# Kernel tuning notes

Hardware: AMD Instinct MI355X
Metric: run time of the kernel (lower is better)

The kernel has to match this reference:

```python
import jax, jax.numpy as jnp
import numpy as np

D_MODEL = 1024
NUM_HEADS = 16
HEAD_DIM = D_MODEL // NUM_HEADS  # 64
ROPE_BASE = 10000.0


def setup_inputs() -> dict:
    key = jax.random.key(0)
    ks = jax.random.split(key, 12)
    B, S, D = 4, 2048, D_MODEL
    scale = 1.0 / np.sqrt(D)
    inp = {
        'query': jax.random.normal(ks[0], (B, S, D), jnp.float32),
        'key': jax.random.normal(ks[1], (B, S, D), jnp.float32),
        'value': jax.random.normal(ks[2], (B, S, D), jnp.float32),
        'Wq': jax.random.normal(ks[3], (D, D), jnp.float32) * scale,
        'bq': jnp.zeros((D,), jnp.float32),
        'Wk': jax.random.normal(ks[4], (D, D), jnp.float32) * scale,
        'bk': jnp.zeros((D,), jnp.float32),
        'Wv': jax.random.normal(ks[5], (D, D), jnp.float32) * scale,
        'bv': jnp.zeros((D,), jnp.float32),
        'Wo': jax.random.normal(ks[6], (D, D), jnp.float32) * scale,
        'bo': jnp.zeros((D,), jnp.float32),
    }
    return inp


def _rope_cos_sin(seq_len, head_dim, dtype):
    inv_freq = 1.0 / (ROPE_BASE ** (jnp.arange(0, head_dim, 2, dtype=jnp.float32) / head_dim))
    t = jnp.arange(seq_len, dtype=jnp.float32)
    freqs = jnp.einsum('i,j->ij', t, inv_freq)          # [S, hd/2]
    emb = jnp.concatenate([freqs, freqs], axis=-1)      # [S, hd]
    return jnp.cos(emb).astype(dtype), jnp.sin(emb).astype(dtype)


def _rotate_half(x):
    x1, x2 = jnp.split(x, 2, axis=-1)
    return jnp.concatenate([-x2, x1], axis=-1)


def reference(query, key, value, Wq, bq, Wk, bk, Wv, bv, Wo, bo):
    B, T, D = query.shape
    H, hd = NUM_HEADS, HEAD_DIM
    # projections -> [B, H, S, hd]
    Q = (query @ Wq + bq).reshape(B, T, H, hd).transpose(0, 2, 1, 3)
    K = (key @ Wk + bk).reshape(B, -1, H, hd).transpose(0, 2, 1, 3)
    V = (value @ Wv + bv).reshape(B, -1, H, hd).transpose(0, 2, 1, 3)
    # RoPE
    cos, sin = _rope_cos_sin(T, hd, Q.dtype)            # [S, hd]
    Q = Q * cos + _rotate_half(Q) * sin
    K = K * cos + _rotate_half(K) * sin
    # attention
    scores = jnp.einsum('bhtd,bhsd->bhts', Q, K) / jnp.sqrt(jnp.asarray(hd, Q.dtype))
    attn = jax.nn.softmax(scores, axis=-1)
    context = jnp.einsum('bhts,bhsd->bhtd', attn, V)
    context = context.transpose(0, 2, 1, 3).reshape(B, T, D)
    return context @ Wo + bo
```

## Files before the change

### kernel.cpp

```cpp
#include <hip/hip_runtime.h>
#include <hip/hip_bf16.h>
#include <cstdint>
#include <cstddef>

typedef __bf16 bf16_t;
typedef __bf16 bf16x8 __attribute__((ext_vector_type(8)));
typedef __bf16 bf16x4v __attribute__((ext_vector_type(4)));
typedef __bf16 bf16x2v __attribute__((ext_vector_type(2)));
typedef float f32x4 __attribute__((ext_vector_type(4)));
typedef float f32x16 __attribute__((ext_vector_type(16)));
typedef uint32_t u32x4 __attribute__((ext_vector_type(4)));
typedef uint32_t u32x2 __attribute__((ext_vector_type(2)));

#define DEVI static __device__ __forceinline__

DEVI void gl_lds16(const void* g, void* l) {
    __builtin_amdgcn_global_load_lds((const __attribute__((address_space(1))) void*)g,
                                     (__attribute__((address_space(3))) void*)l, 16, 0, 0);
}

DEVI float fexp2(float x) {
#if __has_builtin(__builtin_amdgcn_exp2f)
    return __builtin_amdgcn_exp2f(x);
#else
    return __expf(x * 0.6931471805599453f);
#endif
}

DEVI uint32_t pkbf16(float a, float b) {
    bf16x2v t;
    t[0] = (bf16_t)a;
    t[1] = (bf16_t)b;
    return __builtin_bit_cast(uint32_t, t);
}

__global__ __launch_bounds__(256) void castk(const float* __restrict__ i0, const float* __restrict__ i1,
                                             const float* __restrict__ i2, bf16_t* __restrict__ o0,
                                             bf16_t* __restrict__ o1, bf16_t* __restrict__ o2) {
    const float* in = blockIdx.y == 0 ? i0 : blockIdx.y == 1 ? i1 : i2;
    bf16_t* out = blockIdx.y == 0 ? o0 : blockIdx.y == 1 ? o1 : o2;
    size_t i = ((size_t)blockIdx.x * 256 + threadIdx.x) * 4;
    float4 v = *(const float4*)(in + i);
    bf16x4v o;
    o[0] = (bf16_t)v.x; o[1] = (bf16_t)v.y; o[2] = (bf16_t)v.z; o[3] = (bf16_t)v.w;
    *(bf16x4v*)(out + i) = o;
}

__global__ __launch_bounds__(256) void wtrans(const float* __restrict__ W0, const float* __restrict__ W1,
                                              const float* __restrict__ W2, const float* __restrict__ W3,
                                              bf16_t* __restrict__ O0, bf16_t* __restrict__ O1,
                                              bf16_t* __restrict__ O2, bf16_t* __restrict__ O3) {
    const float* W; bf16_t* O;
    switch (blockIdx.z) {
        case 0: W = W0; O = O0; break;
        case 1: W = W1; O = O1; break;
        case 2: W = W2; O = O2; break;
        default: W = W3; O = O3; break;
    }
    __shared__ float t[32][33];
    int tx = threadIdx.x & 31, ty = threadIdx.x >> 5;
    int bx = blockIdx.x * 32, by = blockIdx.y * 32;
#pragma unroll
    for (int yy = 0; yy < 4; ++yy)
        t[ty + yy * 8][tx] = W[(size_t)(by + ty + yy * 8) * 1024 + bx + tx];
    __syncthreads();
#pragma unroll
    for (int yy = 0; yy < 4; ++yy)
        O[(size_t)(bx + ty + yy * 8) * 1024 + by + tx] = (bf16_t)t[tx][ty + yy * 8];
}

__global__ __launch_bounds__(256) void rope_tab(float* __restrict__ ctab, float* __restrict__ stab) {
    int idx = blockIdx.x * 256 + threadIdx.x;
    int s = idx >> 5, i = idx & 31;
    float inv = 1.0f / powf(10000.0f, (float)i * (1.0f / 32.0f));
    float f = (float)s * inv;
    ctab[idx] = cosf(f);
    stab[idx] = sinf(f);
}

__global__ __launch_bounds__(256) void gemm_qkv(const bf16_t* __restrict__ Xq, const bf16_t* __restrict__ Xk,
                                                const bf16_t* __restrict__ Xv, const bf16_t* __restrict__ Wqt,
                                                const bf16_t* __restrict__ Wkt, const bf16_t* __restrict__ Wvt,
                                                const float* __restrict__ bqp, const float* __restrict__ bkp,
                                                const float* __restrict__ bvp, bf16_t* __restrict__ Qo,
                                                bf16_t* __restrict__ Ko, bf16_t* __restrict__ Vo,
                                                const float* __restrict__ ctab, const float* __restrict__ stab) {
    constexpr int K = 1024;
    const int z = blockIdx.z;
    const bf16_t* A  = z == 0 ? Xq : z == 1 ? Xk : Xv;
    const bf16_t* Bt = z == 0 ? Wqt : z == 1 ? Wkt : Wvt;
    const float* bias = z == 0 ? bqp : z == 1 ? bkp : bvp;
    bf16_t* O = z == 0 ? Qo : z == 1 ? Ko : Vo;
    const float scale = z == 0 ? 0.18033688011112042f : 1.0f;

    __shared__ alignas(16) bf16_t As[128 * 64];
    __shared__ alignas(16) bf16_t Bs[128 * 64];
    const int tid = threadIdx.x;
    const int w = tid >> 6, lane = tid & 63, c = lane & 15, qd = lane >> 4;
    const int wm = w >> 1, wn = w & 1;
    const int c7 = c & 7;
    const int m0 = blockIdx.x * 128, n0 = blockIdx.y * 128;
    f32x4 acc[4][4] = {};
    for (int kt = 0; kt < K / 64; ++kt) {
#pragma unroll
        for (int l = 0; l < 4; ++l) {
            int slot = l * 256 + tid;
            int row = slot >> 3, ch = slot & 7;
            int sch = ch ^ (row & 7);
            gl_lds16(A + (size_t)(m0 + row) * K + kt * 64 + sch * 8, (char*)As + (size_t)slot * 16);
            gl_lds16(Bt + (size_t)(n0 + row) * K + kt * 64 + sch * 8, (char*)Bs + (size_t)slot * 16);
        }
        __syncthreads();
#pragma unroll
        for (int kk = 0; kk < 2; ++kk) {
            const int cs8 = (kk * 4 + qd) ^ c7;
            bf16x8 af[4], bfr[4];
#pragma unroll
            for (int i = 0; i < 4; ++i)
                af[i] = *(const bf16x8*)&As[(wm * 64 + i * 16 + c) * 64 + cs8 * 8];
#pragma unroll
            for (int j = 0; j < 4; ++j)
                bfr[j] = *(const bf16x8*)&Bs[(wn * 64 + j * 16 + c) * 64 + cs8 * 8];
#pragma unroll
            for (int i = 0; i < 4; ++i)
#pragma unroll
                for (int j = 0; j < 4; ++j)
                    acc[i][j] = __builtin_amdgcn_mfma_f32_16x16x32_bf16(af[i], bfr[j], acc[i][j], 0, 0, 0);
        }
        __syncthreads();
    }
    const int mb = m0 + wm * 64;
    const int nb = n0 + wn * 64;
    const int h = nb >> 6;
    if (z == 2) {
#pragma unroll
        for (int i = 0; i < 4; ++i) {
            int m = mb + i * 16 + qd * 4;
            int b = m >> 11, s = m & 2047;
#pragma unroll
            for (int j = 0; j < 4; ++j) {
                int d = j * 16 + c;
                float bv = bias[nb + d];
                bf16x4v v4;
#pragma unroll
                for (int r = 0; r < 4; ++r) v4[r] = (bf16_t)(acc[i][j][r] + bv);
                *(bf16x4v*)(O + ((size_t)(b * 16 + h) * 64 + d) * 2048 + s) = v4;
            }
        }
    } else {
#pragma unroll
        for (int i = 0; i < 4; ++i)
#pragma unroll
            for (int jh = 0; jh < 2; ++jh) {
                int d1 = jh * 16 + c;
                float b1 = bias[nb + d1];
                float b2 = bias[nb + d1 + 32];
#pragma unroll
                for (int r = 0; r < 4; ++r) {
                    int m = mb + i * 16 + qd * 4 + r;
                    int b = m >> 11, s = m & 2047;
                    float v1 = acc[i][jh][r] + b1;
                    float v2 = acc[i][jh + 2][r] + b2;
                    float ct = ctab[s * 32 + d1];
                    float st = stab[s * 32 + d1];
                    size_t base = ((size_t)(b * 16 + h) * 2048 + s) * 64;
                    O[base + d1]      = (bf16_t)((v1 * ct - v2 * st) * scale);
                    O[base + d1 + 32] = (bf16_t)((v2 * ct + v1 * st) * scale);
                }
            }
    }
}

__global__ __launch_bounds__(256) void gemm_out(const bf16_t* __restrict__ A, const bf16_t* __restrict__ Bt,
                                                const float* __restrict__ bias, float* __restrict__ O) {
    constexpr int K = 1024, N = 1024;
    __shared__ alignas(16) bf16_t As[128 * 64];
    __shared__ alignas(16) bf16_t Bs[128 * 64];
    const int tid = threadIdx.x;
    const int w = tid >> 6, lane = tid & 63, c = lane & 15, qd = lane >> 4;
    const int wm = w >> 1, wn = w & 1;
    const int c7 = c & 7;
    const int m0 = blockIdx.x * 128, n0 = blockIdx.y * 128;
    f32x4 acc[4][4] = {};
    for (int kt = 0; kt < K / 64; ++kt) {
#pragma unroll
        for (int l = 0; l < 4; ++l) {
            int slot = l * 256 + tid;
            int row = slot >> 3, ch = slot & 7;
            int sch = ch ^ (row & 7);
            gl_lds16(A + (size_t)(m0 + row) * K + kt * 64 + sch * 8, (char*)As + (size_t)slot * 16);
            gl_lds16(Bt + (size_t)(n0 + row) * K + kt * 64 + sch * 8, (char*)Bs + (size_t)slot * 16);
        }
        __syncthreads();
#pragma unroll
        for (int kk = 0; kk < 2; ++kk) {
            const int cs8 = (kk * 4 + qd) ^ c7;
            bf16x8 af[4], bfr[4];
#pragma unroll
            for (int i = 0; i < 4; ++i)
                af[i] = *(const bf16x8*)&As[(wm * 64 + i * 16 + c) * 64 + cs8 * 8];
#pragma unroll
            for (int j = 0; j < 4; ++j)
                bfr[j] = *(const bf16x8*)&Bs[(wn * 64 + j * 16 + c) * 64 + cs8 * 8];
#pragma unroll
            for (int i = 0; i < 4; ++i)
#pragma unroll
                for (int j = 0; j < 4; ++j)
                    acc[i][j] = __builtin_amdgcn_mfma_f32_16x16x32_bf16(af[i], bfr[j], acc[i][j], 0, 0, 0);
        }
        __syncthreads();
    }
    const int mb = m0 + wm * 64, nb = n0 + wn * 64;
#pragma unroll
    for (int i = 0; i < 4; ++i)
#pragma unroll
        for (int j = 0; j < 4; ++j) {
            int n = nb + j * 16 + c;
            float bv = bias[n];
#pragma unroll
            for (int r = 0; r < 4; ++r) {
                int m = mb + i * 16 + qd * 4 + r;
                O[(size_t)m * N + n] = acc[i][j][r] + bv;
            }
        }
}

__global__ __launch_bounds__(256, 4) void attn(const bf16_t* __restrict__ Q, const bf16_t* __restrict__ K,
                                               const bf16_t* __restrict__ Vt, bf16_t* __restrict__ ctx) {
    constexpr int S = 2048;
    __shared__ alignas(16) char smem[32768];
    const int tid = threadIdx.x, w = tid >> 6, lane = tid & 63;
    const int lo5 = lane & 31, hi = lane >> 5;
    const int rm = (lo5 >> 1) & 7;
    const int bh = blockIdx.x, q0 = blockIdx.y * 128;
    const bf16_t* Qb = Q + (size_t)bh * S * 64 + (size_t)q0 * 64;
    const bf16_t* Kb = K + (size_t)bh * S * 64;
    const bf16_t* Vb = Vt + (size_t)bh * 64 * S;
#pragma unroll
    for (int l = 0; l < 4; ++l) {
        int slot = l * 256 + tid;
        int row = slot >> 3, ch = slot & 7;
        int sch = ch ^ ((row >> 1) & 7);
        gl_lds16(Qb + (size_t)row * 64 + sch * 8, smem + (size_t)slot * 16);
    }
    __syncthreads();
    bf16x8 qf[4];
    {
        const bf16_t* Qs = (const bf16_t*)smem;
#pragma unroll
        for (int kc = 0; kc < 4; ++kc)
            qf[kc] = *(const bf16x8*)&Qs[(size_t)(w * 32 + lo5) * 64 + ((kc * 2 + hi) ^ rm) * 8];
    }
    __syncthreads();
    auto stageKV = [&](int kt, int buf) {
        const int s0 = kt * 64;
        char* kbase = smem + buf * 16384;
        char* vbase = kbase + 8192;
#pragma unroll
        for (int l = 0; l < 2; ++l) {
            int slot = l * 256 + tid;
            int row = slot >> 3, ch = slot & 7;
            int sch = ch ^ ((row >> 1) & 7);
            gl_lds16(Kb + (size_t)(s0 + row) * 64 + sch * 8, kbase + (size_t)slot * 16);
            gl_lds16(Vb + (size_t)row * S + s0 + sch * 8, vbase + (size_t)slot * 16);
        }
    };
    stageKV(0, 0);
    f32x16 acc_o[2] = {};
    f32x16 acc_l = {};
    const f32x16 Z16 = {};
    bf16x8 ones;
    {
        u32x4 ov = {0x3F803F80u, 0x3F803F80u, 0x3F803F80u, 0x3F803F80u};
        ones = __builtin_bit_cast(bf16x8, ov);
    }
    __syncthreads();
    for (int kt = 0; kt < S / 64; ++kt) {
        const int cur = kt & 1;
        if (kt + 1 < S / 64) stageKV(kt + 1, cur ^ 1);
        const bf16_t* KsC = (const bf16_t*)(smem + cur * 16384);
        const bf16_t* VsC = (const bf16_t*)(smem + cur * 16384 + 8192);
        f32x16 st[2];
#pragma unroll
        for (int kc = 0; kc < 4; ++kc) {
            bf16x8 kf[2];
#pragma unroll
            for (int sb = 0; sb < 2; ++sb)
                kf[sb] = *(const bf16x8*)&KsC[(size_t)(sb * 32 + lo5) * 64 + ((kc * 2 + hi) ^ rm) * 8];
#pragma unroll
            for (int sb = 0; sb < 2; ++sb)
                st[sb] = __builtin_amdgcn_mfma_f32_32x32x16_bf16(kf[sb], qf[kc],
                                                                 kc == 0 ? Z16 : st[sb], 0, 0, 0);
        }
        uint32_t pku[2][8];
#pragma unroll
        for (int sb = 0; sb < 2; ++sb)
#pragma unroll
            for (int u = 0; u < 8; ++u)
                pku[sb][u] = pkbf16(fexp2(st[sb][2 * u]), fexp2(st[sb][2 * u + 1]));
#pragma unroll
        for (int skc = 0; skc < 4; ++skc) {
            bf16x8 vf[2];
#pragma unroll
            for (int db = 0; db < 2; ++db)
                vf[db] = *(const bf16x8*)&VsC[(size_t)(db * 32 + lo5) * 64 + ((skc * 2 + hi) ^ rm) * 8];
            const int sb = skc >> 1, b = (skc & 1) * 4;
            uint32_t p0 = pku[sb][b + 0], p1 = pku[sb][b + 1];
            uint32_t p2 = pku[sb][b + 2], p3 = pku[sb][b + 3];
#if __has_builtin(__builtin_amdgcn_permlane32_swap)
            u32x2 r02 = __builtin_amdgcn_permlane32_swap(p0, p2, false, false);
            u32x2 r13 = __builtin_amdgcn_permlane32_swap(p1, p3, false, false);
            u32x4 av = {r02[0], r13[0], r02[1], r13[1]};
#else
            uint32_t send0 = hi ? p0 : p2;
            uint32_t send1 = hi ? p1 : p3;
            uint32_t recv0 = __shfl_xor(send0, 32);
            uint32_t recv1 = __shfl_xor(send1, 32);
            u32x4 av = {hi ? recv0 : p0, hi ? recv1 : p1,
                        hi ? p2 : recv0, hi ? p3 : recv1};
#endif
            bf16x8 af = __builtin_bit_cast(bf16x8, av);
            acc_l = __builtin_amdgcn_mfma_f32_32x32x16_bf16(af, ones, acc_l, 0, 0, 0);
#pragma unroll
            for (int db = 0; db < 2; ++db)
                acc_o[db] = __builtin_amdgcn_mfma_f32_32x32x16_bf16(af, vf[db], acc_o[db], 0, 0, 0);
        }
        __syncthreads();
    }
    const int b = bh >> 4, h = bh & 15;
    float linv[16];
#pragma unroll
    for (int r = 0; r < 16; ++r) linv[r] = 1.0f / acc_l[r];
#pragma unroll
    for (int db = 0; db < 2; ++db)
#pragma unroll
        for (int r = 0; r < 16; ++r) {
            int qrow = q0 + w * 32 + (r & 3) + 8 * (r >> 2) + 4 * hi;
            int d = db * 32 + lo5;
            float o = acc_o[db][r] * linv[r];
            ctx[((size_t)(b * 2048 + qrow)) * 1024 + (size_t)h * 64 + d] = (bf16_t)o;
        }
}

extern "C" void kernel_launch(void* const* d_in, const int* in_sizes, int n_in,
                              void* d_out, int out_size, void* d_ws, size_t ws_size,
                              hipStream_t stream) {
    (void)in_sizes; (void)n_in; (void)out_size; (void)ws_size;
    const float* query = (const float*)d_in[0];
    const float* key   = (const float*)d_in[1];
    const float* value = (const float*)d_in[2];
    const float* Wq = (const float*)d_in[3];
    const float* bq = (const float*)d_in[4];
    const float* Wk = (const float*)d_in[5];
    const float* bk = (const float*)d_in[6];
    const float* Wv = (const float*)d_in[7];
    const float* bv = (const float*)d_in[8];
    const float* Wo = (const float*)d_in[9];
    const float* bo = (const float*)d_in[10];

    const size_t SZ = (size_t)8192 * 1024;
    bf16_t* Xq = (bf16_t*)d_ws;
    bf16_t* Xk = Xq + SZ;
    bf16_t* Xv = Xk + SZ;
    bf16_t* Qb = Xv + SZ;
    bf16_t* Kb = Qb + SZ;
    bf16_t* Vtb = Kb + SZ;
    bf16_t* Wqt = Vtb + SZ;
    bf16_t* Wkt = Wqt + 1024 * 1024;
    bf16_t* Wvt = Wkt + 1024 * 1024;
    bf16_t* Wot = Wvt + 1024 * 1024;
    float* ctab = (float*)(Wot + 1024 * 1024);
    float* stab = ctab + 2048 * 32;
    bf16_t* CT = Xq;

    castk<<<dim3(8192, 3), 256, 0, stream>>>(query, key, value, Xq, Xk, Xv);
    wtrans<<<dim3(32, 32, 4), 256, 0, stream>>>(Wq, Wk, Wv, Wo, Wqt, Wkt, Wvt, Wot);
    rope_tab<<<256, 256, 0, stream>>>(ctab, stab);
    gemm_qkv<<<dim3(64, 8, 3), 256, 0, stream>>>(Xq, Xk, Xv, Wqt, Wkt, Wvt, bq, bk, bv,
                                                 Qb, Kb, Vtb, ctab, stab);
    attn<<<dim3(64, 16), 256, 0, stream>>>(Qb, Kb, Vtb, CT);
    gemm_out<<<dim3(64, 8), 256, 0, stream>>>(CT, Wot, bo, (float*)d_out);
}
```

Before: 340.4 us.

## Software-pipeline attention loop to overlap QK^T of next tile with PV of previous

Restructures the attention inner loop into a skewed pipeline: each window computes the QK^T scores and exp for tile i while doing the PV and row-sum MFMAs for tile i-1, using ping-pong packed-probability register arrays. K and V staging are split into separate double buffers so K is prefetched one tile ahead and V is loaded one tile later. The goal is to interleave exp/VALU work with MFMA work and hide LDS latency. It costs more live registers (two pku arrays) and adds a drain iteration, which could hurt occupancy under the 4-wave launch bound.

```diff
diff --git a/kernel.cpp b/kernel.cpp
--- a/kernel.cpp
+++ b/kernel.cpp
@@ -227,7 +227,7 @@
 
 __global__ __launch_bounds__(256, 4) void attn(const bf16_t* __restrict__ Q, const bf16_t* __restrict__ K,
                                                const bf16_t* __restrict__ Vt, bf16_t* __restrict__ ctx) {
-    constexpr int S = 2048;
+    constexpr int S = 2048, NT = S / 64;
     __shared__ alignas(16) char smem[32768];
     const int tid = threadIdx.x, w = tid >> 6, lane = tid & 63;
     const int lo5 = lane & 31, hi = lane >> 5;
@@ -252,20 +252,28 @@
             qf[kc] = *(const bf16x8*)&Qs[(size_t)(w * 32 + lo5) * 64 + ((kc * 2 + hi) ^ rm) * 8];
     }
     __syncthreads();
-    auto stageKV = [&](int kt, int buf) {
+    auto stageK = [&](int kt, int buf) {
         const int s0 = kt * 64;
-        char* kbase = smem + buf * 16384;
-        char* vbase = kbase + 8192;
+        char* kbase = smem + buf * 8192;
 #pragma unroll
         for (int l = 0; l < 2; ++l) {
             int slot = l * 256 + tid;
             int row = slot >> 3, ch = slot & 7;
             int sch = ch ^ ((row >> 1) & 7);
             gl_lds16(Kb + (size_t)(s0 + row) * 64 + sch * 8, kbase + (size_t)slot * 16);
+        }
+    };
+    auto stageV = [&](int kt, int buf) {
+        const int s0 = kt * 64;
+        char* vbase = smem + 16384 + buf * 8192;
+#pragma unroll
+        for (int l = 0; l < 2; ++l) {
+            int slot = l * 256 + tid;
+            int row = slot >> 3, ch = slot & 7;
+            int sch = ch ^ ((row >> 1) & 7);
             gl_lds16(Vb + (size_t)row * S + s0 + sch * 8, vbase + (size_t)slot * 16);
         }
     };
-    stageKV(0, 0);
     f32x16 acc_o[2] = {};
     f32x16 acc_l = {};
     const f32x16 Z16 = {};
@@ -274,59 +282,69 @@
         u32x4 ov = {0x3F803F80u, 0x3F803F80u, 0x3F803F80u, 0x3F803F80u};
         ones = __builtin_bit_cast(bf16x8, ov);
     }
+    stageK(0, 0);
     __syncthreads();
-    for (int kt = 0; kt < S / 64; ++kt) {
-        const int cur = kt & 1;
-        if (kt + 1 < S / 64) stageKV(kt + 1, cur ^ 1);
-        const bf16_t* KsC = (const bf16_t*)(smem + cur * 16384);
-        const bf16_t* VsC = (const bf16_t*)(smem + cur * 16384 + 8192);
+    uint32_t pkuA[2][8] = {}, pkuB[2][8] = {};
+    auto window = [&](int wi, uint32_t (&pkuP)[2][8], uint32_t (&pkuN)[2][8]) {
+        if (wi + 1 < NT) stageK(wi + 1, (wi + 1) & 1);
+        if (wi < NT) stageV(wi, wi & 1);
         f32x16 st[2];
-#pragma unroll
-        for (int kc = 0; kc < 4; ++kc) {
-            bf16x8 kf[2];
-#pragma unroll
-            for (int sb = 0; sb < 2; ++sb)
-                kf[sb] = *(const bf16x8*)&KsC[(size_t)(sb * 32 + lo5) * 64 + ((kc * 2 + hi) ^ rm) * 8];
-#pragma unroll
-            for (int sb = 0; sb < 2; ++sb)
-                st[sb] = __builtin_amdgcn_mfma_f32_32x32x16_bf16(kf[sb], qf[kc],
-                                                                 kc == 0 ? Z16 : st[sb], 0, 0, 0);
-        }
-        uint32_t pku[2][8];
-#pragma unroll
-        for (int sb = 0; sb < 2; ++sb)
-#pragma unroll
-            for (int u = 0; u < 8; ++u)
-                pku[sb][u] = pkbf16(fexp2(st[sb][2 * u]), fexp2(st[sb][2 * u + 1]));
+        if (wi < NT) {
+            const bf16_t* KsC = (const bf16_t*)(smem + (wi & 1) * 8192);
+#pragma unroll
+            for (int kc = 0; kc < 4; ++kc) {
+                bf16x8 kf[2];
+#pragma unroll
+                for (int sb = 0; sb < 2; ++sb)
+                    kf[sb] = *(const bf16x8*)&KsC[(size_t)(sb * 32 + lo5) * 64 + ((kc * 2 + hi) ^ rm) * 8];
+#pragma unroll
+                for (int sb = 0; sb < 2; ++sb)
+                    st[sb] = __builtin_amdgcn_mfma_f32_32x32x16_bf16(kf[sb], qf[kc],
+                                                                     kc == 0 ? Z16 : st[sb], 0, 0, 0);
+            }
+        }
+        const bf16_t* VsC = (const bf16_t*)(smem + 16384 + ((wi - 1) & 1) * 8192);
 #pragma unroll
         for (int skc = 0; skc < 4; ++skc) {
-            bf16x8 vf[2];
-#pragma unroll
-            for (int db = 0; db < 2; ++db)
-                vf[db] = *(const bf16x8*)&VsC[(size_t)(db * 32 + lo5) * 64 + ((skc * 2 + hi) ^ rm) * 8];
             const int sb = skc >> 1, b = (skc & 1) * 4;
-            uint32_t p0 = pku[sb][b + 0], p1 = pku[sb][b + 1];
-            uint32_t p2 = pku[sb][b + 2], p3 = pku[sb][b + 3];
+            if (wi < NT) {
+#pragma unroll
+                for (int u = 0; u < 4; ++u)
+                    pkuN[sb][b + u] = pkbf16(fexp2(st[sb][2 * (b + u)]), fexp2(st[sb][2 * (b + u) + 1]));
+            }
+            if (wi >= 1) {
+                bf16x8 vf[2];
+#pragma unroll
+                for (int db = 0; db < 2; ++db)
+                    vf[db] = *(const bf16x8*)&VsC[(size_t)(db * 32 + lo5) * 64 + ((skc * 2 + hi) ^ rm) * 8];
+                uint32_t p0 = pkuP[sb][b + 0], p1 = pkuP[sb][b + 1];
+                uint32_t p2 = pkuP[sb][b + 2], p3 = pkuP[sb][b + 3];
 #if __has_builtin(__builtin_amdgcn_permlane32_swap)
-            u32x2 r02 = __builtin_amdgcn_permlane32_swap(p0, p2, false, false);
-            u32x2 r13 = __builtin_amdgcn_permlane32_swap(p1, p3, false, false);
-            u32x4 av = {r02[0], r13[0], r02[1], r13[1]};
+                u32x2 r02 = __builtin_amdgcn_permlane32_swap(p0, p2, false, false);
+                u32x2 r13 = __builtin_amdgcn_permlane32_swap(p1, p3, false, false);
+                u32x4 av = {r02[0], r13[0], r02[1], r13[1]};
 #else
-            uint32_t send0 = hi ? p0 : p2;
-            uint32_t send1 = hi ? p1 : p3;
-            uint32_t recv0 = __shfl_xor(send0, 32);
-            uint32_t recv1 = __shfl_xor(send1, 32);
-            u32x4 av = {hi ? recv0 : p0, hi ? recv1 : p1,
-                        hi ? p2 : recv0, hi ? p3 : recv1};
+                uint32_t send0 = hi ? p0 : p2;
+                uint32_t send1 = hi ? p1 : p3;
+                uint32_t recv0 = __shfl_xor(send0, 32);
+                uint32_t recv1 = __shfl_xor(send1, 32);
+                u32x4 av = {hi ? recv0 : p0, hi ? recv1 : p1,
+                            hi ? p2 : recv0, hi ? p3 : recv1};
 #endif
-            bf16x8 af = __builtin_bit_cast(bf16x8, av);
-            acc_l = __builtin_amdgcn_mfma_f32_32x32x16_bf16(af, ones, acc_l, 0, 0, 0);
-#pragma unroll
-            for (int db = 0; db < 2; ++db)
-                acc_o[db] = __builtin_amdgcn_mfma_f32_32x32x16_bf16(af, vf[db], acc_o[db], 0, 0, 0);
+                bf16x8 af = __builtin_bit_cast(bf16x8, av);
+                acc_l = __builtin_amdgcn_mfma_f32_32x32x16_bf16(af, ones, acc_l, 0, 0, 0);
+#pragma unroll
+                for (int db = 0; db < 2; ++db)
+                    acc_o[db] = __builtin_amdgcn_mfma_f32_32x32x16_bf16(af, vf[db], acc_o[db], 0, 0, 0);
+            }
         }
         __syncthreads();
-    }
+    };
+    for (int wi = 0; wi < NT; wi += 2) {
+        window(wi, pkuB, pkuA);
+        window(wi + 1, pkuA, pkuB);
+    }
+    window(NT, pkuB, pkuA);
     const int b = bh >> 4, h = bh & 15;
     float linv[16];
 #pragma unroll
```

Result: slower. 387.7 us (+13.9%).
